# Kernel optimization log

Measured on AMD Instinct MI355X. Metric: run time of the kernel, lower is better.

## Reference

```python
import jax, jax.numpy as jnp
import numpy as np
from math import pi, log

B, H, W, C = 8, 128, 128, 3
N_LAT, D_LAT = 256, 512
DEPTH = 4
NUM_BANDS = 6
MAX_FREQ = 10.0
BASE = 2.0
CROSS_HEADS, CROSS_DH = 1, 64
LAT_HEADS, LAT_DH = 8, 64
FF_MULT = 4
INPUT_DIM = 2 * (2 * NUM_BANDS + 1) + C  # 29


def setup_inputs():
    ki = iter(jax.random.split(jax.random.key(0), 40))

    def nrm(shape, s=0.02):
        return jax.random.normal(next(ki), shape, jnp.float32) * s

    ic, il = CROSS_HEADS * CROSS_DH, LAT_HEADS * LAT_DH
    d, q = DEPTH, INPUT_DIM
    return {
        "x": jax.random.normal(next(ki), (B, D_LAT), jnp.float32),
        "latents": jax.random.normal(next(ki), (N_LAT, D_LAT), jnp.float32),
        "W_l2l": nrm((D_LAT, N_LAT * D_LAT)),
        "b_l2l": jnp.zeros((N_LAT * D_LAT,), jnp.float32),
        "ca_ln_q_g": jnp.ones((d, q)), "ca_ln_q_b": jnp.zeros((d, q)),
        "ca_ln_c_g": jnp.ones((d, D_LAT)), "ca_ln_c_b": jnp.zeros((d, D_LAT)),
        "ca_Wq": nrm((d, q, ic)), "ca_Wkv": nrm((d, D_LAT, 2 * ic)),
        "ca_Wo": nrm((d, ic, q)), "ca_bo": jnp.zeros((d, q)),
        "cf_ln_g": jnp.ones((d, q)), "cf_ln_b": jnp.zeros((d, q)),
        "cf_W1": nrm((d, q, q * FF_MULT * 2)), "cf_b1": jnp.zeros((d, q * FF_MULT * 2)),
        "cf_W2": nrm((d, q * FF_MULT, q)), "cf_b2": jnp.zeros((d, q)),
        "la_ln_g": jnp.ones((d, D_LAT)), "la_ln_b": jnp.zeros((d, D_LAT)),
        "la_Wq": nrm((d, D_LAT, il)), "la_Wkv": nrm((d, D_LAT, 2 * il)),
        "la_Wo": nrm((d, il, D_LAT)), "la_bo": jnp.zeros((d, D_LAT)),
        "lf_ln_g": jnp.ones((d, D_LAT)), "lf_ln_b": jnp.zeros((d, D_LAT)),
        "lf_W1": nrm((d, D_LAT, D_LAT * FF_MULT * 2)), "lf_b1": jnp.zeros((d, D_LAT * FF_MULT * 2)),
        "lf_W2": nrm((d, D_LAT * FF_MULT, D_LAT)), "lf_b2": jnp.zeros((d, D_LAT)),
    }


def _ln(t, g, b):
    m = jnp.mean(t, -1, keepdims=True)
    v = jnp.mean(jnp.square(t - m), -1, keepdims=True)
    return (t - m) * jax.lax.rsqrt(v + 1e-5) * g + b


def _attn(xq, ctx, Wq, Wkv, Wo, bo, heads):
    dh = Wq.shape[-1] // heads
    b, n, _ = xq.shape
    m = ctx.shape[1]
    qh = (xq @ Wq).reshape(b, n, heads, dh)
    k, v = jnp.split(ctx @ Wkv, 2, axis=-1)
    kh = k.reshape(b, m, heads, dh)
    vh = v.reshape(b, m, heads, dh)
    sim = jnp.einsum('bihd,bjhd->bhij', qh, kh) * (dh ** -0.5)
    attn = jax.nn.softmax(sim, axis=-1)
    out = jnp.einsum('bhij,bjhd->bihd', attn, vh).reshape(b, n, heads * dh)
    return out @ Wo + bo


def _geglu_ff(t, W1, b1, W2, b2):
    a, g = jnp.split(t @ W1 + b1, 2, axis=-1)
    return (a * jax.nn.gelu(g, approximate=False)) @ W2 + b2


def _forward(x, latents, W_l2l, b_l2l, ca_ln_q_g, ca_ln_q_b, ca_ln_c_g, ca_ln_c_b,
             ca_Wq, ca_Wkv, ca_Wo, ca_bo, cf_ln_g, cf_ln_b, cf_W1, cf_b1, cf_W2, cf_b2,
             la_ln_g, la_ln_b, la_Wq, la_Wkv, la_Wo, la_bo,
             lf_ln_g, lf_ln_b, lf_W1, lf_b1, lf_W2, lf_b2):
    # expand latent code to a set of latents and add learned latent array
    lat = (x @ W_l2l + b_l2l).reshape(B, N_LAT, D_LAT) + latents  # (B, N, D)

    # Fourier positional encoding of the output grid
    pos = jnp.stack(jnp.meshgrid(jnp.linspace(-1.0, 1.0, H), jnp.linspace(-1.0, 1.0, W), indexing='ij'), axis=-1)  # (H, W, 2)
    scales = BASE ** jnp.linspace(1.0, log(MAX_FREQ / 2) / log(BASE), NUM_BANDS)  # torch.logspace
    xp = pos[..., None] * scales * pi  # (H, W, 2, NUM_BANDS)
    enc = jnp.concatenate([jnp.sin(xp), jnp.cos(xp), pos[..., None]], axis=-1)  # (H, W, 2, 2B+1)
    enc = enc.reshape(H, W, 2 * (2 * NUM_BANDS + 1)).astype(jnp.float32)

    data = jnp.concatenate([jnp.zeros((B, H, W, C), jnp.float32),
                            jnp.broadcast_to(enc, (B, H, W, enc.shape[-1]))], axis=-1)
    data = data.reshape(B, H * W, INPUT_DIM)

    for i in range(DEPTH):
        ln_lat = _ln(lat, la_ln_g[i], la_ln_b[i])
        lat = lat + _attn(ln_lat, ln_lat, la_Wq[i], la_Wkv[i], la_Wo[i], la_bo[i], LAT_HEADS)
        lat = lat + _geglu_ff(_ln(lat, lf_ln_g[i], lf_ln_b[i]), lf_W1[i], lf_b1[i], lf_W2[i], lf_b2[i])
        qn = _ln(data, ca_ln_q_g[i], ca_ln_q_b[i])
        cn = _ln(lat, ca_ln_c_g[i], ca_ln_c_b[i])
        data = data + _attn(qn, cn, ca_Wq[i], ca_Wkv[i], ca_Wo[i], ca_bo[i], CROSS_HEADS)
        data = data + _geglu_ff(_ln(data, cf_ln_g[i], cf_ln_b[i]), cf_W1[i], cf_b1[i], cf_W2[i], cf_b2[i])

    return data[..., :C].reshape(B, H, W, C)


def reference(x, latents, W_l2l, b_l2l, ca_ln_q_g, ca_ln_q_b, ca_ln_c_g, ca_ln_c_b,
              ca_Wq, ca_Wkv, ca_Wo, ca_bo, cf_ln_g, cf_ln_b, cf_W1, cf_b1, cf_W2, cf_b2,
              la_ln_g, la_ln_b, la_Wq, la_Wkv, la_Wo, la_bo,
              lf_ln_g, lf_ln_b, lf_W1, lf_b1, lf_W2, lf_b2):
    return _forward(x, latents, W_l2l, b_l2l, ca_ln_q_g, ca_ln_q_b, ca_ln_c_g, ca_ln_c_b,
                    ca_Wq, ca_Wkv, ca_Wo, ca_bo, cf_ln_g, cf_ln_b, cf_W1, cf_b1, cf_W2, cf_b2,
                    la_ln_g, la_ln_b, la_Wq, la_Wkv, la_Wo, la_bo,
                    lf_ln_g, lf_ln_b, lf_W1, lf_b1, lf_W2, lf_b2)
```

## Files before the change

kernel.cpp:

```cpp
#include <hip/hip_runtime.h>
#include <math.h>

#define DEV __device__ __forceinline__
#define LSTRIDE 8537088

DEV float gelu_exact(float x){ return 0.5f*x*(1.0f+erff(x*0.70710678118654752440f)); }

DEV unsigned short f2bf(float x){
  union { float f; unsigned int u; } v; v.f = x;
  unsigned int r = v.u + 0x7FFFu + ((v.u >> 16) & 1u);
  return (unsigned short)(r >> 16);
}
DEV float bf2f(unsigned short b){ union { unsigned int u; float f; } v; v.u = ((unsigned int)b)<<16; return v.f; }
DEV void split2(float x, unsigned short& h, unsigned short& l){
  h = f2bf(x); l = f2bf(x - bf2f(h));
}

typedef __bf16 bf16x8 __attribute__((ext_vector_type(8)));
typedef float  f32x4  __attribute__((ext_vector_type(4)));

DEV void gload16(const void* g, void* lds){
  __builtin_amdgcn_global_load_lds((const __attribute__((address_space(1))) unsigned int*)g,
                                   (__attribute__((address_space(3))) unsigned int*)lds, 16, 0, 0);
}

__global__ __launch_bounds__(256) void k_encode(float* __restrict__ data)
{
  int p = blockIdx.x*256 + threadIdx.x;
  int hh = p >> 7, ww = p & 127;
  float y = -1.0f + hh*(2.0f/127.0f);
  float x = -1.0f + ww*(2.0f/127.0f);
  float e[26];
  #pragma unroll
  for (int i=0;i<6;i++){
    float sc = exp2f(1.0f + i*0.26438561897747245f) * 3.14159265358979323846f;
    e[i]     = sinf(y*sc);
    e[6+i]   = cosf(y*sc);
    e[13+i]  = sinf(x*sc);
    e[19+i]  = cosf(x*sc);
  }
  e[12]=y; e[25]=x;
  #pragma unroll
  for (int b=0;b<8;b++){
    float* dr = data + ((size_t)(b*16384 + p))*29;
    dr[0]=0.f; dr[1]=0.f; dr[2]=0.f;
    #pragma unroll
    for (int c=0;c<26;c++) dr[3+c]=e[c];
  }
}

__global__ __launch_bounds__(256) void k_l2l(const float* __restrict__ x,
    const float* __restrict__ Wl, const float* __restrict__ bl,
    const float* __restrict__ latents, float* __restrict__ lat)
{
  __shared__ float xs[8*512];
  int tid = threadIdx.x;
  for (int idx=tid; idx<4096; idx+=256) xs[idx]=x[idx];
  __syncthreads();
  int nIdx = blockIdx.x*256 + tid;
  float acc[8] = {0,0,0,0,0,0,0,0};
  for (int k=0;k<512;k++){
    float w = Wl[(size_t)k*131072 + nIdx];
    #pragma unroll
    for (int m=0;m<8;m++) acc[m] += xs[m*512+k]*w;
  }
  float add = bl[nIdx] + latents[nIdx];
  #pragma unroll
  for (int m=0;m<8;m++) lat[(size_t)m*131072 + nIdx] = acc[m] + add;
}

__global__ __launch_bounds__(256) void k_ln512s(const float* __restrict__ X,
    const float* __restrict__ g, const float* __restrict__ bv,
    unsigned short* __restrict__ hi, unsigned short* __restrict__ lo)
{
  __shared__ float red[8];
  int row = blockIdx.x, tid = threadIdx.x;
  const float* x = X + (size_t)row*512;
  float v0 = x[tid], v1 = x[tid+256];
  float s = v0+v1;
  #pragma unroll
  for (int off=32; off; off>>=1) s += __shfl_xor(s, off);
  if ((tid&63)==0) red[tid>>6] = s;
  __syncthreads();
  float mean = (red[0]+red[1]+red[2]+red[3]) * (1.0f/512.0f);
  float d0 = v0-mean, d1 = v1-mean;
  float q = d0*d0 + d1*d1;
  #pragma unroll
  for (int off=32; off; off>>=1) q += __shfl_xor(q, off);
  if ((tid&63)==0) red[4+(tid>>6)] = q;
  __syncthreads();
  float var = (red[4]+red[5]+red[6]+red[7]) * (1.0f/512.0f);
  float rstd = rsqrtf(var + 1e-5f);
  float y0 = d0*rstd*g[tid]     + bv[tid];
  float y1 = d1*rstd*g[tid+256] + bv[tid+256];
  unsigned short h,l;
  split2(y0,h,l); hi[(size_t)row*512+tid]=h;     lo[(size_t)row*512+tid]=l;
  split2(y1,h,l); hi[(size_t)row*512+tid+256]=h; lo[(size_t)row*512+tid+256]=l;
}

__global__ __launch_bounds__(256) void k_split_w(const float* __restrict__ W,
    unsigned short* __restrict__ hi, int K, int N)
{
  __shared__ float t[64][65];
  int z = blockIdx.z;
  W  += (size_t)z*K*N;
  hi += (size_t)z*LSTRIDE;
  unsigned short* lo = hi + (size_t)N*K;
  int k0 = blockIdx.x*64, n0 = blockIdx.y*64;
  int tid = threadIdx.x;
  #pragma unroll
  for (int i=0;i<4;i++){
    int s = tid + 256*i;
    int r = s >> 4, c4 = (s & 15)*4;
    float4 v = *(const float4*)&W[(size_t)(k0+r)*N + n0 + c4];
    t[r][c4+0]=v.x; t[r][c4+1]=v.y; t[r][c4+2]=v.z; t[r][c4+3]=v.w;
  }
  __syncthreads();
  #pragma unroll
  for (int i=0;i<4;i++){
    int s = tid + 256*i;
    int n = s >> 4, kc = (s & 15)*4;
    size_t o = (size_t)(n0+n)*K + k0 + kc;
    #pragma unroll
    for (int j=0;j<4;j++){
      unsigned short h,l; split2(t[kc+j][n], h, l);
      hi[o+j]=h; lo[o+j]=l;
    }
  }
}

__global__ __launch_bounds__(256) void k_prep_t(const float* __restrict__ src,
    unsigned short* __restrict__ dst, int K, int N, int Kd, int Nd)
{
  int z = blockIdx.z;
  src += (size_t)z*K*N;
  dst += (size_t)z*LSTRIDE;
  for (int idx = blockIdx.x*256 + threadIdx.x; idx < Nd*Kd; idx += gridDim.x*256){
    int n = idx / Kd, k = idx - n*Kd;
    float v = (k<K && n<N) ? src[(size_t)k*N + n] : 0.f;
    dst[idx] = f2bf(v);
  }
}

__global__ __launch_bounds__(256) void k_prep_w1(const float* __restrict__ W1,
    const float* __restrict__ b1, unsigned short* __restrict__ dst)
{
  int z = blockIdx.z;
  W1  += (size_t)z*6728;
  b1  += (size_t)z*232;
  dst += (size_t)z*LSTRIDE;
  float* b1r = (float*)(dst + 8192);
  for (int idx = blockIdx.x*256 + threadIdx.x; idx < 256*32; idx += gridDim.x*256){
    int n = idx >> 5, k = idx & 31;
    int f = n & 127, isg = n >> 7;
    float v = 0.f;
    if (f < 116 && k < 29) v = W1[(size_t)k*232 + isg*116 + f];
    dst[idx] = f2bf(v);
  }
  int n = blockIdx.x*256 + threadIdx.x;
  if (n < 256){
    int f = n & 127, isg = n >> 7;
    b1r[n] = (f < 116) ? b1[isg*116 + f] : 0.f;
  }
}

__global__ __launch_bounds__(256) void k_mfma(
    const unsigned short* __restrict__ Ahi, const unsigned short* __restrict__ Bhi,
    const float* __restrict__ bias, float* __restrict__ C,
    int M, int N, int K, int Ksplit, int accum)
{
  __shared__ unsigned short sm[4*128*32];
  int tid = threadIdx.x, lane = tid & 63, w = tid >> 6;
  int bm = blockIdx.x*128, bn = blockIdx.y*128;
  int Ks = K / Ksplit;
  int kbeg = blockIdx.z * Ks;
  const unsigned short* tsrc;
  if      (w==0) tsrc = Ahi + (size_t)bm*K;
  else if (w==1) tsrc = Ahi + (size_t)M*K + (size_t)bm*K;
  else if (w==2) tsrc = Bhi + (size_t)bn*K;
  else           tsrc = Bhi + (size_t)N*K + (size_t)bn*K;
  unsigned short* mylds = sm + w*4096;
  f32x4 acc[4][4];
  #pragma unroll
  for(int i=0;i<4;i++)
    #pragma unroll
    for(int j=0;j<4;j++) acc[i][j] = (f32x4){0.f,0.f,0.f,0.f};
  int wm = (w>>1)*64, wn = (w&1)*64;
  int frow = lane & 15, fq = lane >> 4;
  for (int k0 = kbeg; k0 < kbeg + Ks; k0 += 32){
    #pragma unroll
    for (int j=0;j<8;j++){
      int idx = j*64 + lane;
      int row = idx >> 2, qp = idx & 3;
      int q = (qp - row) & 3;
      gload16(tsrc + (size_t)row*K + k0 + q*8, mylds + j*512);
    }
    __syncthreads();
    bf16x8 ah[4], al[4];
    #pragma unroll
    for (int mt=0;mt<4;mt++){
      int row = wm + mt*16 + frow;
      int off = row*32 + ((fq + row)&3)*8;
      ah[mt] = *(const bf16x8*)(sm + off);
      al[mt] = *(const bf16x8*)(sm + 4096 + off);
    }
    #pragma unroll
    for (int nt=0;nt<4;nt++){
      int rowb = wn + nt*16 + frow;
      int offb = rowb*32 + ((fq + rowb)&3)*8;
      bf16x8 bh = *(const bf16x8*)(sm + 2*4096 + offb);
      bf16x8 bl = *(const bf16x8*)(sm + 3*4096 + offb);
      #pragma unroll
      for (int mt=0;mt<4;mt++){
        acc[mt][nt] = __builtin_amdgcn_mfma_f32_16x16x32_bf16(ah[mt], bh, acc[mt][nt], 0,0,0);
        acc[mt][nt] = __builtin_amdgcn_mfma_f32_16x16x32_bf16(ah[mt], bl, acc[mt][nt], 0,0,0);
        acc[mt][nt] = __builtin_amdgcn_mfma_f32_16x16x32_bf16(al[mt], bh, acc[mt][nt], 0,0,0);
      }
    }
    __syncthreads();
  }
  size_t zoff = (size_t)blockIdx.z * ((size_t)M*N);
  #pragma unroll
  for (int mt=0;mt<4;mt++){
    #pragma unroll
    for (int nt=0;nt<4;nt++){
      int col = bn + wn + nt*16 + frow;
      float bv = (bias && blockIdx.z==0) ? bias[col] : 0.f;
      #pragma unroll
      for (int r=0;r<4;r++){
        int row = bm + wm + mt*16 + fq*4 + r;
        float v = acc[mt][nt][r] + bv;
        if (accum) atomicAdd(&C[(size_t)row*N + col], v);
        else       C[zoff + (size_t)row*N + col] = v;
      }
    }
  }
}

__global__ __launch_bounds__(256) void k_mfma_glu(
    const unsigned short* __restrict__ Ahi, const unsigned short* __restrict__ Whi,
    const float* __restrict__ b1, unsigned short* __restrict__ Ghi,
    unsigned short* __restrict__ Glo)
{
  __shared__ unsigned short sm[16384];
  int tid = threadIdx.x, lane = tid & 63, w = tid >> 6;
  int bm = blockIdx.x*128, bnp = blockIdx.y*64;
  const unsigned short* Alo = Ahi + (size_t)2048*512;
  const unsigned short* Wlo = Whi + (size_t)4096*512;
  f32x4 aa[4][2], ag[4][2];
  #pragma unroll
  for (int i=0;i<4;i++)
    #pragma unroll
    for (int j=0;j<2;j++){ aa[i][j]=(f32x4){0.f,0.f,0.f,0.f}; ag[i][j]=(f32x4){0.f,0.f,0.f,0.f}; }
  int wm = (w>>1)*64, wnp = (w&1)*32;
  int frow = lane & 15, fq = lane >> 4;
  for (int k0=0;k0<512;k0+=32){
    #pragma unroll
    for (int j=0;j<8;j++){
      int c0 = w*512 + j*64;
      int c  = c0 + lane;
      int sel = c0 >> 8;
      const unsigned short* src; int wi;
      if (sel < 4){
        src = (sel < 2 ? Ahi : Alo) + (size_t)bm*512;
        wi = c & 511;
      } else {
        const unsigned short* wb = (sel < 6) ? Whi : Wlo;
        int cb = bnp + ((sel & 1) ? 2048 : 0);
        src = wb + (size_t)cb*512;
        wi = c & 255;
      }
      int row = wi >> 2, qp = wi & 3;
      int q = (qp - row) & 3;
      gload16(src + (size_t)row*512 + k0 + q*8, sm + c0*8);
    }
    __syncthreads();
    bf16x8 ah[4], al[4];
    #pragma unroll
    for (int mt=0;mt<4;mt++){
      int r = wm + mt*16 + frow;
      int off = r*32 + ((fq + r)&3)*8;
      ah[mt] = *(const bf16x8*)(sm + off);
      al[mt] = *(const bf16x8*)(sm + 4096 + off);
    }
    #pragma unroll
    for (int nt=0;nt<2;nt++){
      int rb = wnp + nt*16 + frow;
      int offb = rb*32 + ((fq + rb)&3)*8;
      bf16x8 bah = *(const bf16x8*)(sm +  8192 + offb);
      bf16x8 bgh = *(const bf16x8*)(sm + 10240 + offb);
      bf16x8 bal = *(const bf16x8*)(sm + 12288 + offb);
      bf16x8 bgl = *(const bf16x8*)(sm + 14336 + offb);
      #pragma unroll
      for (int mt=0;mt<4;mt++){
        aa[mt][nt] = __builtin_amdgcn_mfma_f32_16x16x32_bf16(ah[mt], bah, aa[mt][nt], 0,0,0);
        aa[mt][nt] = __builtin_amdgcn_mfma_f32_16x16x32_bf16(ah[mt], bal, aa[mt][nt], 0,0,0);
        aa[mt][nt] = __builtin_amdgcn_mfma_f32_16x16x32_bf16(al[mt], bah, aa[mt][nt], 0,0,0);
        ag[mt][nt] = __builtin_amdgcn_mfma_f32_16x16x32_bf16(ah[mt], bgh, ag[mt][nt], 0,0,0);
        ag[mt][nt] = __builtin_amdgcn_mfma_f32_16x16x32_bf16(ah[mt], bgl, ag[mt][nt], 0,0,0);
        ag[mt][nt] = __builtin_amdgcn_mfma_f32_16x16x32_bf16(al[mt], bgh, ag[mt][nt], 0,0,0);
      }
    }
    __syncthreads();
  }
  #pragma unroll
  for (int mt=0;mt<4;mt++){
    #pragma unroll
    for (int nt=0;nt<2;nt++){
      int col = bnp + wnp + nt*16 + frow;
      float ba = b1[col], bg = b1[2048+col];
      #pragma unroll
      for (int r=0;r<4;r++){
        int row = bm + wm + mt*16 + fq*4 + r;
        float av = aa[mt][nt][r] + ba;
        float gv = ag[mt][nt][r] + bg;
        unsigned short h,l; split2(av*gelu_exact(gv), h, l);
// ... 54 lines not shown
      for (int j=0;j<8;j++) v[j] = (__bf16)qp[kt*32 + j];
      aq[kt]=v;
    }
  } else {
    const unsigned short* qp = (const unsigned short*)Qv + (size_t)qrow*q_rs + h*64 + g*8;
    aq[0] = *(const bf16x8*)(qp);
    aq[1] = *(const bf16x8*)(qp + 32);
  }
  const unsigned short* kbb = Kb + ((size_t)bh*256 + l15)*64 + g*8;
  f32x4 sc[16];
  #pragma unroll
  for (int nt=0;nt<16;nt++) sc[nt] = (f32x4){0.f,0.f,0.f,0.f};
  #pragma unroll
  for (int nt=0;nt<16;nt++){
    bf16x8 b0 = *(const bf16x8*)(kbb + (size_t)nt*1024);
    bf16x8 b1 = *(const bf16x8*)(kbb + (size_t)nt*1024 + 32);
    sc[nt] = __builtin_amdgcn_mfma_f32_16x16x32_bf16(aq[0], b0, sc[nt], 0,0,0);
    sc[nt] = __builtin_amdgcn_mfma_f32_16x16x32_bf16(aq[1], b1, sc[nt], 0,0,0);
  }
  float mx[4] = {-1e30f,-1e30f,-1e30f,-1e30f};
  #pragma unroll
  for (int nt=0;nt<16;nt++)
    #pragma unroll
    for (int r=0;r<4;r++){ float v = sc[nt][r]*scale; sc[nt][r]=v; mx[r]=fmaxf(mx[r],v); }
  #pragma unroll
  for (int r=0;r<4;r++){
    #pragma unroll
    for (int m=1;m<16;m<<=1) mx[r] = fmaxf(mx[r], __shfl_xor(mx[r], m));
  }
  float sum[4] = {0.f,0.f,0.f,0.f};
  #pragma unroll
  for (int nt=0;nt<16;nt++)
    #pragma unroll
    for (int r=0;r<4;r++){ float e = __expf(sc[nt][r]-mx[r]); sc[nt][r]=e; sum[r]+=e; }
  #pragma unroll
  for (int r=0;r<4;r++){
    #pragma unroll
    for (int m=1;m<16;m<<=1) sum[r] += __shfl_xor(sum[r], m);
  }
  f32x4 o[4];
  #pragma unroll
  for (int nd=0;nd<4;nd++) o[nd] = (f32x4){0.f,0.f,0.f,0.f};
  unsigned short* pw = Pw + w*640;
  const unsigned short* vb  = Vthi + ((size_t)bh*64 + l15)*256 + g*8;
  const unsigned short* vbl = SPLITV ? (Vtlo + ((size_t)bh*64 + l15)*256 + g*8) : (const unsigned short*)0;
  #pragma unroll
  for (int kt=0;kt<8;kt++){
    __builtin_amdgcn_wave_barrier();
    #pragma unroll
    for (int t2=0;t2<2;t2++){
      int nt = kt*2 + t2;
      #pragma unroll
      for (int r=0;r<4;r++)
        pw[(g*4+r)*40 + t2*16 + l15] = f2bf(sc[nt][r]);
    }
    __builtin_amdgcn_wave_barrier();
    bf16x8 ap = *(const bf16x8*)(pw + l15*40 + g*8);
    #pragma unroll
    for (int nd=0;nd<4;nd++){
      bf16x8 bv = *(const bf16x8*)(vb + (size_t)nd*4096 + kt*32);
      o[nd] = __builtin_amdgcn_mfma_f32_16x16x32_bf16(ap, bv, o[nd], 0,0,0);
      if (SPLITV){
        bf16x8 bl = *(const bf16x8*)(vbl + (size_t)nd*4096 + kt*32);
        o[nd] = __builtin_amdgcn_mfma_f32_16x16x32_bf16(ap, bl, o[nd], 0,0,0);
      }
    }
  }
  float inv[4];
  #pragma unroll
  for (int r=0;r<4;r++) inv[r] = 1.0f/sum[r];
  int orow0 = b*nper + q0;
  #pragma unroll
  for (int nd=0;nd<4;nd++){
    #pragma unroll
    for (int r=0;r<4;r++){
      float v = o[nd][r]*inv[r];
      size_t off = (size_t)(orow0 + g*4 + r)*o_rs + h*64 + nd*16 + l15;
      if (OSPLIT){ unsigned short hh,ll; split2(v,hh,ll); O0[off]=hh; O1[off]=ll; }
      else O0[off] = f2bf(v);
    }
  }
}

__global__ __launch_bounds__(256) void k_qproj_f(const float* __restrict__ X,
    const float* __restrict__ lng, const float* __restrict__ lnb,
    const unsigned short* __restrict__ Wt, unsigned short* __restrict__ Out)
{
  __shared__ __align__(16) unsigned short sm[128*40];
  int tid = threadIdx.x;
  int row0b = blockIdx.x*128;
  if (tid < 128){
    const float* x = X + (size_t)(row0b + tid)*29;
    float a[29]; float s = 0.f;
    #pragma unroll
    for (int k=0;k<29;k++){ a[k]=x[k]; s+=a[k]; }
    float mean = s*(1.0f/29.0f);
    float qv = 0.f;
    #pragma unroll
    for (int k=0;k<29;k++){ float d=a[k]-mean; qv+=d*d; }
    float rstd = rsqrtf(qv*(1.0f/29.0f) + 1e-5f);
    unsigned short yb[32] __attribute__((aligned(16)));
    #pragma unroll
    for (int k=0;k<29;k++) yb[k] = f2bf((a[k]-mean)*rstd*lng[k] + lnb[k]);
    yb[29]=0; yb[30]=0; yb[31]=0;
    uint4* d4 = (uint4*)(sm + tid*40);
    const uint4* s4 = (const uint4*)yb;
    d4[0]=s4[0]; d4[1]=s4[1]; d4[2]=s4[2]; d4[3]=s4[3];
  }
  __syncthreads();
  int lane = tid & 63, w = tid >> 6;
  int l15 = lane & 15, gq = lane >> 4;
  int rw = w*32;
  bf16x8 a0 = *(const bf16x8*)(sm + (rw + l15)*40 + gq*8);
  bf16x8 a1 = *(const bf16x8*)(sm + (rw + 16 + l15)*40 + gq*8);
  f32x4 acc[2][4];
  #pragma unroll
  for (int mt=0;mt<2;mt++)
    #pragma unroll
    for (int nt=0;nt<4;nt++) acc[mt][nt] = (f32x4){0.f,0.f,0.f,0.f};
  #pragma unroll
  for (int nt=0;nt<4;nt++){
    bf16x8 bw = *(const bf16x8*)(Wt + (size_t)(nt*16 + l15)*32 + gq*8);
    acc[0][nt] = __builtin_amdgcn_mfma_f32_16x16x32_bf16(a0, bw, acc[0][nt], 0,0,0);
    acc[1][nt] = __builtin_amdgcn_mfma_f32_16x16x32_bf16(a1, bw, acc[1][nt], 0,0,0);
  }
  #pragma unroll
  for (int mt=0;mt<2;mt++)
    #pragma unroll
    for (int nt=0;nt<4;nt++)
      #pragma unroll
      for (int r=0;r<4;r++)
        Out[(size_t)(row0b + rw + mt*16 + gq*4 + r)*64 + nt*16 + l15] = f2bf(acc[mt][nt][r]);
}

__global__ __launch_bounds__(256) void k_nsmall(const unsigned short* __restrict__ A,
    const unsigned short* __restrict__ Wt, const float* __restrict__ bias,
    float* __restrict__ C, int K)
{
  int tid = threadIdx.x, lane = tid & 63, w = tid >> 6;
  int l15 = lane & 15, g = lane >> 4;
  int row0 = blockIdx.x*128 + w*32;
  f32x4 acc[2][2];
  #pragma unroll
  for (int mt=0;mt<2;mt++)
    #pragma unroll
    for (int nt=0;nt<2;nt++) acc[mt][nt] = (f32x4){0.f,0.f,0.f,0.f};
  for (int kt=0; kt<K; kt+=32){
    bf16x8 a0 = *(const bf16x8*)(A + (size_t)(row0 + l15)*K + kt + g*8);
    bf16x8 a1 = *(const bf16x8*)(A + (size_t)(row0 + 16 + l15)*K + kt + g*8);
    #pragma unroll
    for (int nt=0;nt<2;nt++){
      bf16x8 bw = *(const bf16x8*)(Wt + (size_t)(nt*16 + l15)*K + kt + g*8);
      acc[0][nt] = __builtin_amdgcn_mfma_f32_16x16x32_bf16(a0, bw, acc[0][nt], 0,0,0);
      acc[1][nt] = __builtin_amdgcn_mfma_f32_16x16x32_bf16(a1, bw, acc[1][nt], 0,0,0);
    }
  }
  #pragma unroll
  for (int mt=0;mt<2;mt++)
    #pragma unroll
    for (int nt=0;nt<2;nt++){
      int col = nt*16 + l15;
      if (col < 29){
        #pragma unroll
        for (int r=0;r<4;r++){
          size_t off = (size_t)(row0 + mt*16 + g*4 + r)*29 + col;
          C[off] += acc[mt][nt][r] + bias[col];
        }
      }
    }
}

__global__ __launch_bounds__(256) void k_ff1_f(const float* __restrict__ X,
    const float* __restrict__ lng, const float* __restrict__ lnb,
    const unsigned short* __restrict__ Wt, const float* __restrict__ b1r,
    unsigned short* __restrict__ G)
{
  __shared__ __align__(16) unsigned short sm[128*40];
  int tid = threadIdx.x;
  int row0b = blockIdx.x*128;
  if (tid < 128){
    const float* x = X + (size_t)(row0b + tid)*29;
    float a[29]; float s = 0.f;
    #pragma unroll
    for (int k=0;k<29;k++){ a[k]=x[k]; s+=a[k]; }
    float mean = s*(1.0f/29.0f);
    float qv = 0.f;
    #pragma unroll
    for (int k=0;k<29;k++){ float d=a[k]-mean; qv+=d*d; }
    float rstd = rsqrtf(qv*(1.0f/29.0f) + 1e-5f);
    unsigned short yb[32] __attribute__((aligned(16)));
    #pragma unroll
    for (int k=0;k<29;k++) yb[k] = f2bf((a[k]-mean)*rstd*lng[k] + lnb[k]);
    yb[29]=0; yb[30]=0; yb[31]=0;
    uint4* d4 = (uint4*)(sm + tid*40);
    const uint4* s4 = (const uint4*)yb;
    d4[0]=s4[0]; d4[1]=s4[1]; d4[2]=s4[2]; d4[3]=s4[3];
  }
  __syncthreads();
  int lane = tid & 63, w = tid >> 6;
  int l15 = lane & 15, gq = lane >> 4;
  int rw = w*32;
  bf16x8 a0 = *(const bf16x8*)(sm + (rw + l15)*40 + gq*8);
  bf16x8 a1 = *(const bf16x8*)(sm + (rw + 16 + l15)*40 + gq*8);
  f32x4 acc[2][16];
  #pragma unroll
  for (int mt=0;mt<2;mt++)
    #pragma unroll
    for (int nt=0;nt<16;nt++) acc[mt][nt] = (f32x4){0.f,0.f,0.f,0.f};
  #pragma unroll
  for (int nt=0;nt<16;nt++){
    bf16x8 bw = *(const bf16x8*)(Wt + (size_t)(nt*16 + l15)*32 + gq*8);
    acc[0][nt] = __builtin_amdgcn_mfma_f32_16x16x32_bf16(a0, bw, acc[0][nt], 0,0,0);
    acc[1][nt] = __builtin_amdgcn_mfma_f32_16x16x32_bf16(a1, bw, acc[1][nt], 0,0,0);
  }
  #pragma unroll
  for (int mt=0;mt<2;mt++){
    #pragma unroll
    for (int t=0;t<8;t++){
      float ba = b1r[t*16 + l15];
      float bg = b1r[128 + t*16 + l15];
      #pragma unroll
      for (int r=0;r<4;r++){
        float av = acc[mt][t][r]   + ba;
        float gv = acc[mt][t+8][r] + bg;
        G[(size_t)(row0b + rw + mt*16 + gq*4 + r)*128 + t*16 + l15] = f2bf(av * gelu_exact(gv));
      }
    }
  }
}

__global__ __launch_bounds__(256) void k_out(const float* __restrict__ data, float* __restrict__ out)
{
  int idx = blockIdx.x*256 + threadIdx.x;
  int p = idx/3, c = idx - p*3;
  out[idx] = data[(size_t)p*29 + c];
}

extern "C" void kernel_launch(void* const* d_in, const int* in_sizes, int n_in,
                              void* d_out, int out_size, void* d_ws, size_t ws_size,
                              hipStream_t stream) {
  const float* x        = (const float*)d_in[0];
  const float* latents  = (const float*)d_in[1];
  const float* W_l2l    = (const float*)d_in[2];
  const float* b_l2l    = (const float*)d_in[3];
  const float* ca_ln_q_g= (const float*)d_in[4];
  const float* ca_ln_q_b= (const float*)d_in[5];
  const float* ca_ln_c_g= (const float*)d_in[6];
  const float* ca_ln_c_b= (const float*)d_in[7];
  const float* ca_Wq    = (const float*)d_in[8];
  const float* ca_Wkv   = (const float*)d_in[9];
  const float* ca_Wo    = (const float*)d_in[10];
  const float* ca_bo    = (const float*)d_in[11];
  const float* cf_ln_g  = (const float*)d_in[12];
  const float* cf_ln_b  = (const float*)d_in[13];
  const float* cf_W1    = (const float*)d_in[14];
  const float* cf_b1    = (const float*)d_in[15];
  const float* cf_W2    = (const float*)d_in[16];
  const float* cf_b2    = (const float*)d_in[17];
  const float* la_ln_g  = (const float*)d_in[18];
  const float* la_ln_b  = (const float*)d_in[19];
  const float* la_Wq    = (const float*)d_in[20];
  const float* la_Wkv   = (const float*)d_in[21];
  const float* la_Wo    = (const float*)d_in[22];
  const float* la_bo    = (const float*)d_in[23];
  const float* lf_ln_g  = (const float*)d_in[24];
  const float* lf_ln_b  = (const float*)d_in[25];
  const float* lf_W1    = (const float*)d_in[26];
  const float* lf_b1    = (const float*)d_in[27];
  const float* lf_W2    = (const float*)d_in[28];
  const float* lf_b2    = (const float*)d_in[29];

  float* ws = (float*)d_ws;
  float* data = ws;
  float* lat  = ws + 3801088;
  unsigned short* latn_hi = (unsigned short*)(ws + 4849664);
  unsigned short* latn_lo = latn_hi + 1048576;
  float* I    = ws + 5898240;
  float* kv_c = ws + 20578304;
  unsigned short* Kb_c = (unsigned short*)(ws + 21626880);
  unsigned short* Vt_c = Kb_c + 131072;
  unsigned short* wsp  = (unsigned short*)(ws + 21757952);
  float* q_l  = I;
  float* kv_l = I + 1048576;
  unsigned short* Kb_l   = (unsigned short*)(I + 3145728);
  unsigned short* Vthi_l = Kb_l + 1048576;
  unsigned short* Vtlo_l = Vthi_l + 1048576;
  unsigned short* ao_hi  = (unsigned short*)(I + 4718592);
  unsigned short* ao_lo  = ao_hi + 1048576;
  unsigned short* gg_hi = (unsigned short*)(I + 8388608);
  unsigned short* gg_lo = gg_hi + 4194304;
  unsigned short* q_c  = (unsigned short*)(I + 2097152);
  unsigned short* gg_c = (unsigned short*)(I + 6291456);

  k_encode<<<64, 256, 0, stream>>>(data);
  k_l2l   <<<512, 256, 0, stream>>>(x, W_l2l, b_l2l, latents, lat);

  k_split_w<<<dim3(8,8,4),  256,0,stream>>>(la_Wq,  wsp,          512, 512);
  k_split_w<<<dim3(8,16,4), 256,0,stream>>>(la_Wkv, wsp+524288,   512, 1024);
  k_split_w<<<dim3(8,8,4),  256,0,stream>>>(la_Wo,  wsp+1572864,  512, 512);
  k_split_w<<<dim3(8,64,4), 256,0,stream>>>(lf_W1,  wsp+2097152,  512, 4096);
  k_split_w<<<dim3(32,8,4), 256,0,stream>>>(lf_W2,  wsp+6291456,  2048, 512);
  k_split_w<<<dim3(8,2,4),  256,0,stream>>>(ca_Wkv, wsp+8388608,  512, 128);
  k_prep_t <<<dim3(4,1,4),256,0,stream>>>(ca_Wq, wsp+8519680, 29, 64, 32, 64);
  k_prep_t <<<dim3(4,1,4),256,0,stream>>>(ca_Wo, wsp+8521728, 64, 29, 64, 32);
  k_prep_t <<<dim3(8,1,4),256,0,stream>>>(cf_W2, wsp+8523776, 116, 29, 128, 32);
  k_prep_w1<<<dim3(32,1,4),256,0,stream>>>(cf_W1, cf_b1, wsp+8527872);

  for (int i=0;i<4;i++){
    unsigned short* wl = wsp + (size_t)i*LSTRIDE;
    unsigned short* wqt  = wl;
    unsigned short* wkvt = wl + 524288;
    unsigned short* wot  = wl + 1572864;
    unsigned short* w1t  = wl + 2097152;
    unsigned short* w2t  = wl + 6291456;
    unsigned short* cakvt= wl + 8388608;
    unsigned short* WqT  = wl + 8519680;
    unsigned short* WoT  = wl + 8521728;
    unsigned short* W2T  = wl + 8523776;
    unsigned short* W1rT = wl + 8527872;
    float* b1r = (float*)(wl + 8536064);

    k_ln512s<<<2048,256,0,stream>>>(lat, la_ln_g+i*512, la_ln_b+i*512, latn_hi, latn_lo);
    k_mfma<<<dim3(16,4,1),256,0,stream>>>(latn_hi, wqt,  nullptr, q_l,  2048, 512, 512, 1, 0);
    k_mfma<<<dim3(16,8,1),256,0,stream>>>(latn_hi, wkvt, nullptr, kv_l, 2048,1024, 512, 1, 0);
    k_kvprep<<<1024,256,0,stream>>>(kv_l, 1024, 0, 512, 8, 64, Kb_l, Vthi_l, Vtlo_l, 1, 0);
    k_attn_mf<1,1,1><<<256,256,0,stream>>>(q_l, Kb_l, Vthi_l, Vtlo_l, ao_hi, ao_lo,
                                           512, 512, 8, 256, 0.125f);
    k_mfma<<<dim3(16,4,2),256,0,stream>>>(ao_hi, wot, la_bo+i*512, lat, 2048, 512, 512, 2, 1);
    k_ln512s<<<2048,256,0,stream>>>(lat, lf_ln_g+i*512, lf_ln_b+i*512, latn_hi, latn_lo);
    k_mfma_glu<<<dim3(16,32),256,0,stream>>>(latn_hi, w1t, lf_b1+i*4096, gg_hi, gg_lo);
    k_mfma<<<dim3(16,4,4),256,0,stream>>>(gg_hi, w2t, lf_b2+i*512, lat, 2048, 512, 2048, 4, 1);
    k_ln512s<<<2048,256,0,stream>>>(lat, ca_ln_c_g+i*512, ca_ln_c_b+i*512, latn_hi, latn_lo);
    k_mfma<<<dim3(16,1,4),256,0,stream>>>(latn_hi, cakvt, nullptr, kv_c, 2048, 128, 512, 4, 0);
    k_kvprep<<<512,256,0,stream>>>(kv_c, 128, 0, 64, 1, 8, Kb_c, Vt_c, nullptr, 4, 262144);
    k_qproj_f<<<1024,256,0,stream>>>(data, ca_ln_q_g+i*29, ca_ln_q_b+i*29, WqT, q_c);
    k_attn_mf<0,0,0><<<2048,256,0,stream>>>(q_c, Kb_c, Vt_c, nullptr, q_c, nullptr,
                                            64, 64, 1, 16384, 0.125f);
    k_nsmall<<<1024,256,0,stream>>>(q_c, WoT, ca_bo+i*29, data, 64);
    k_ff1_f<<<1024,256,0,stream>>>(data, cf_ln_g+i*29, cf_ln_b+i*29, W1rT, b1r, gg_c);
    k_nsmall<<<1024,256,0,stream>>>(gg_c, W2T, cf_b2+i*29, data, 128);
  }

  k_out<<<1536,256,0,stream>>>(data, (float*)d_out);
}
```

Before: 1.939 ms.

## Fuse latent QKV projection with KV prep and fuse cross-attention/FF chains

Merges the latent Q and KV weight splits into one contiguous QKV matrix and computes it in a single MFMA kernel whose epilogue writes Q in fp32, K in bf16 and V transposed in split bf16 directly, removing the separate kvprep pass and the fp32 KV intermediate. The cross-attention query LN+projection, attention and output projection are fused into one kernel that keeps intermediates in LDS. The cross feed-forward GEGLU and second projection are fused likewise. This cuts launches and global round trips of intermediates, at the cost of more LDS per block and higher register pressure.

```diff
diff --git a/kernel.cpp b/kernel.cpp
--- a/kernel.cpp
+++ b/kernel.cpp
@@ -99,13 +99,13 @@
 }
 
 __global__ __launch_bounds__(256) void k_split_w(const float* __restrict__ W,
-    unsigned short* __restrict__ hi, int K, int N)
+    unsigned short* __restrict__ hi, int K, int N, int Ntot, int n0off)
 {
   __shared__ float t[64][65];
   int z = blockIdx.z;
   W  += (size_t)z*K*N;
   hi += (size_t)z*LSTRIDE;
-  unsigned short* lo = hi + (size_t)N*K;
+  unsigned short* lo = hi + (size_t)Ntot*K;
   int k0 = blockIdx.x*64, n0 = blockIdx.y*64;
   int tid = threadIdx.x;
   #pragma unroll
@@ -120,7 +120,7 @@
   for (int i=0;i<4;i++){
     int s = tid + 256*i;
     int n = s >> 4, kc = (s & 15)*4;
-    size_t o = (size_t)(n0+n)*K + k0 + kc;
+    size_t o = (size_t)(n0off + n0 + n)*K + k0 + kc;
     #pragma unroll
     for (int j=0;j<4;j++){
       unsigned short h,l; split2(t[kc+j][n], h, l);
@@ -232,6 +232,86 @@
         float v = acc[mt][nt][r] + bv;
         if (accum) atomicAdd(&C[(size_t)row*N + col], v);
         else       C[zoff + (size_t)row*N + col] = v;
+      }
+    }
+  }
+}
+
+__global__ __launch_bounds__(256) void k_mfma_qkv(
+    const unsigned short* __restrict__ Ahi, const unsigned short* __restrict__ Bhi,
+    float* __restrict__ qout, unsigned short* __restrict__ Kb,
+    unsigned short* __restrict__ Vthi, unsigned short* __restrict__ Vtlo,
+    int M, int N, int K)
+{
+  __shared__ unsigned short sm[4*128*32];
+  int tid = threadIdx.x, lane = tid & 63, w = tid >> 6;
+  int bm = blockIdx.x*128, bn = blockIdx.y*128;
+  const unsigned short* tsrc;
+  if      (w==0) tsrc = Ahi + (size_t)bm*K;
+  else if (w==1) tsrc = Ahi + (size_t)M*K + (size_t)bm*K;
+  else if (w==2) tsrc = Bhi + (size_t)bn*K;
+  else           tsrc = Bhi + (size_t)N*K + (size_t)bn*K;
+  unsigned short* mylds = sm + w*4096;
+  f32x4 acc[4][4];
+  #pragma unroll
+  for(int i=0;i<4;i++)
+    #pragma unroll
+    for(int j=0;j<4;j++) acc[i][j] = (f32x4){0.f,0.f,0.f,0.f};
+  int wm = (w>>1)*64, wn = (w&1)*64;
+  int frow = lane & 15, fq = lane >> 4;
+  for (int k0 = 0; k0 < K; k0 += 32){
+    #pragma unroll
+    for (int j=0;j<8;j++){
+      int idx = j*64 + lane;
+      int row = idx >> 2, qp = idx & 3;
+      int q = (qp - row) & 3;
+      gload16(tsrc + (size_t)row*K + k0 + q*8, mylds + j*512);
+    }
+    __syncthreads();
+    bf16x8 ah[4], al[4];
+    #pragma unroll
+    for (int mt=0;mt<4;mt++){
+      int row = wm + mt*16 + frow;
+      int off = row*32 + ((fq + row)&3)*8;
+      ah[mt] = *(const bf16x8*)(sm + off);
+      al[mt] = *(const bf16x8*)(sm + 4096 + off);
+    }
+    #pragma unroll
+    for (int nt=0;nt<4;nt++){
+      int rowb = wn + nt*16 + frow;
+      int offb = rowb*32 + ((fq + rowb)&3)*8;
+      bf16x8 bh = *(const bf16x8*)(sm + 2*4096 + offb);
+      bf16x8 bl = *(const bf16x8*)(sm + 3*4096 + offb);
+      #pragma unroll
+      for (int mt=0;mt<4;mt++){
+        acc[mt][nt] = __builtin_amdgcn_mfma_f32_16x16x32_bf16(ah[mt], bh, acc[mt][nt], 0,0,0);
+        acc[mt][nt] = __builtin_amdgcn_mfma_f32_16x16x32_bf16(ah[mt], bl, acc[mt][nt], 0,0,0);
+        acc[mt][nt] = __builtin_amdgcn_mfma_f32_16x16x32_bf16(al[mt], bh, acc[mt][nt], 0,0,0);
+      }
+    }
+    __syncthreads();
+  }
+  #pragma unroll
+  for (int mt=0;mt<4;mt++){
+    #pragma unroll
+    for (int nt=0;nt<4;nt++){
+      int col = bn + wn + nt*16 + frow;
+      #pragma unroll
+      for (int r=0;r<4;r++){
+        int row = bm + wm + mt*16 + fq*4 + r;
+        float v = acc[mt][nt][r];
+        int b = row >> 8, j = row & 255;
+        if (col < 512){
+          qout[(size_t)row*512 + col] = v;
+        } else if (col < 1024){
+          int kc = col - 512, h = kc >> 6, d = kc & 63;
+          Kb[((size_t)((b*8+h)*256 + j))*64 + d] = f2bf(v);
+        } else {
+          int vc = col - 1024, h = vc >> 6, d = vc & 63;
+          size_t idx = ((size_t)((b*8+h)*64 + d))*256 + j;
+          unsigned short hh,ll; split2(v,hh,ll);
+          Vthi[idx]=hh; Vtlo[idx]=ll;
+        }
       }
     }
   }
@@ -452,12 +532,156 @@
   }
 }
 
-__global__ __launch_bounds__(256) void k_qproj_f(const float* __restrict__ X,
-    const float* __restrict__ lng, const float* __restrict__ lnb,
-    const unsigned short* __restrict__ Wt, unsigned short* __restrict__ Out)
-{
-  __shared__ __align__(16) unsigned short sm[128*40];
-  int tid = threadIdx.x;
+__global__ __launch_bounds__(256) void k_cattn(
+    const float* __restrict__ X, const float* __restrict__ lng, const float* __restrict__ lnb,
+    const unsigned short* __restrict__ WqT, const unsigned short* __restrict__ Kb,
+    const unsigned short* __restrict__ Vt, const unsigned short* __restrict__ WoT,
+    const float* __restrict__ bo, float* __restrict__ C, float scale)
+{
+  __shared__ __align__(16) unsigned short qn[64*40];
+  __shared__ __align__(16) unsigned short qa[4][16*72];
+  int tid = threadIdx.x, lane = tid & 63, w = tid >> 6;
+  int l15 = lane & 15, g = lane >> 4;
+  int r0 = blockIdx.x*64;
+  int bh = r0 >> 14;
+  if (tid < 64){
+    const float* x = X + (size_t)(r0 + tid)*29;
+    float a[29]; float s = 0.f;
+    #pragma unroll
+    for (int k=0;k<29;k++){ a[k]=x[k]; s+=a[k]; }
+    float mean = s*(1.0f/29.0f);
+    float qv = 0.f;
+    #pragma unroll
+    for (int k=0;k<29;k++){ float d=a[k]-mean; qv+=d*d; }
+    float rstd = rsqrtf(qv*(1.0f/29.0f) + 1e-5f);
+    unsigned short yb[32] __attribute__((aligned(16)));
+    #pragma unroll
+    for (int k=0;k<29;k++) yb[k] = f2bf((a[k]-mean)*rstd*lng[k] + lnb[k]);
+    yb[29]=0; yb[30]=0; yb[31]=0;
+    uint4* d4 = (uint4*)(qn + tid*40);
+    const uint4* s4 = (const uint4*)yb;
+    d4[0]=s4[0]; d4[1]=s4[1]; d4[2]=s4[2]; d4[3]=s4[3];
+  }
+  __syncthreads();
+  int rw = w*16;
+  bf16x8 a0 = *(const bf16x8*)(qn + (rw + l15)*40 + g*8);
+  f32x4 qv4[4];
+  #pragma unroll
+  for (int nt=0;nt<4;nt++) qv4[nt] = (f32x4){0.f,0.f,0.f,0.f};
+  #pragma unroll
+  for (int nt=0;nt<4;nt++){
+    bf16x8 bw = *(const bf16x8*)(WqT + (size_t)(nt*16 + l15)*32 + g*8);
+    qv4[nt] = __builtin_amdgcn_mfma_f32_16x16x32_bf16(a0, bw, qv4[nt], 0,0,0);
+  }
+  unsigned short* pa = qa[w];
+  #pragma unroll
+  for (int nt=0;nt<4;nt++)
+    #pragma unroll
+    for (int r=0;r<4;r++)
+      pa[(g*4+r)*72 + nt*16 + l15] = f2bf(qv4[nt][r]);
+  __builtin_amdgcn_wave_barrier();
+  bf16x8 aq[2];
+  aq[0] = *(const bf16x8*)(pa + l15*72 + g*8);
+  aq[1] = *(const bf16x8*)(pa + l15*72 + 32 + g*8);
+  __builtin_amdgcn_wave_barrier();
+  const unsigned short* kbb = Kb + ((size_t)bh*256 + l15)*64 + g*8;
+  f32x4 sc[16];
+  #pragma unroll
+  for (int nt=0;nt<16;nt++) sc[nt] = (f32x4){0.f,0.f,0.f,0.f};
+  #pragma unroll
+  for (int nt=0;nt<16;nt++){
+    bf16x8 b0 = *(const bf16x8*)(kbb + (size_t)nt*1024);
+    bf16x8 b1 = *(const bf16x8*)(kbb + (size_t)nt*1024 + 32);
+    sc[nt] = __builtin_amdgcn_mfma_f32_16x16x32_bf16(aq[0], b0, sc[nt], 0,0,0);
+    sc[nt] = __builtin_amdgcn_mfma_f32_16x16x32_bf16(aq[1], b1, sc[nt], 0,0,0);
+  }
+  float mx[4] = {-1e30f,-1e30f,-1e30f,-1e30f};
+  #pragma unroll
+  for (int nt=0;nt<16;nt++)
+    #pragma unroll
+    for (int r=0;r<4;r++){ float v = sc[nt][r]*scale; sc[nt][r]=v; mx[r]=fmaxf(mx[r],v); }
+  #pragma unroll
+  for (int r=0;r<4;r++){
+    #pragma unroll
+    for (int m=1;m<16;m<<=1) mx[r] = fmaxf(mx[r], __shfl_xor(mx[r], m));
+  }
+  float sum[4] = {0.f,0.f,0.f,0.f};
+  #pragma unroll
+  for (int nt=0;nt<16;nt++)
+    #pragma unroll
+    for (int r=0;r<4;r++){ float e = __expf(sc[nt][r]-mx[r]); sc[nt][r]=e; sum[r]+=e; }
+  #pragma unroll
+  for (int r=0;r<4;r++){
+    #pragma unroll
+    for (int m=1;m<16;m<<=1) sum[r] += __shfl_xor(sum[r], m);
+  }
+  f32x4 o[4];
+  #pragma unroll
+  for (int nd=0;nd<4;nd++) o[nd] = (f32x4){0.f,0.f,0.f,0.f};
+  const unsigned short* vb = Vt + ((size_t)bh*64 + l15)*256 + g*8;
+  #pragma unroll
+  for (int kt=0;kt<8;kt++){
+    __builtin_amdgcn_wave_barrier();
+    #pragma unroll
+    for (int t2=0;t2<2;t2++){
+      int nt = kt*2 + t2;
+      #pragma unroll
+      for (int r=0;r<4;r++)
+        pa[(g*4+r)*40 + t2*16 + l15] = f2bf(sc[nt][r]);
+    }
+    __builtin_amdgcn_wave_barrier();
+    bf16x8 ap = *(const bf16x8*)(pa + l15*40 + g*8);
+    #pragma unroll
+    for (int nd=0;nd<4;nd++){
+      bf16x8 bv = *(const bf16x8*)(vb + (size_t)nd*4096 + kt*32);
+      o[nd] = __builtin_amdgcn_mfma_f32_16x16x32_bf16(ap, bv, o[nd], 0,0,0);
+    }
+  }
+  float inv[4];
+  #pragma unroll
+  for (int r=0;r<4;r++) inv[r] = 1.0f/sum[r];
+  __builtin_amdgcn_wave_barrier();
+  #pragma unroll
+  for (int nd=0;nd<4;nd++)
+    #pragma unroll
+    for (int r=0;r<4;r++)
+      pa[(g*4+r)*72 + nd*16 + l15] = f2bf(o[nd][r]*inv[r]);
+  __builtin_amdgcn_wave_barrier();
+  bf16x8 ao0 = *(const bf16x8*)(pa + l15*72 + g*8);
+  bf16x8 ao1 = *(const bf16x8*)(pa + l15*72 + 32 + g*8);
+  f32x4 c2[2];
+  #pragma unroll
+  for (int nt=0;nt<2;nt++) c2[nt] = (f32x4){0.f,0.f,0.f,0.f};
+  #pragma unroll
+  for (int nt=0;nt<2;nt++){
+    bf16x8 bw0 = *(const bf16x8*)(WoT + (size_t)(nt*16 + l15)*64 + g*8);
+    bf16x8 bw1 = *(const bf16x8*)(WoT + (size_t)(nt*16 + l15)*64 + 32 + g*8);
+    c2[nt] = __builtin_amdgcn_mfma_f32_16x16x32_bf16(ao0, bw0, c2[nt], 0,0,0);
+    c2[nt] = __builtin_amdgcn_mfma_f32_16x16x32_bf16(ao1, bw1, c2[nt], 0,0,0);
+  }
+  #pragma unroll
+  for (int nt=0;nt<2;nt++){
+    int col = nt*16 + l15;
+    if (col < 29){
+      #pragma unroll
+      for (int r=0;r<4;r++){
+        size_t off = (size_t)(r0 + rw + g*4 + r)*29 + col;
+        C[off] += c2[nt][r] + bo[col];
+      }
+    }
+  }
+}
+
+__global__ __launch_bounds__(256) void k_cff(
+    const float* __restrict__ X, const float* __restrict__ lng, const float* __restrict__ lnb,
+    const unsigned short* __restrict__ W1rT, const float* __restrict__ b1r,
+    const unsigned short* __restrict__ W2T, const float* __restrict__ b2,
+    float* __restrict__ C)
+{
+  __shared__ __align__(16) unsigned short sm1[128*40];
+  __shared__ __align__(16) unsigned short gga[4][32*136];
+  int tid = threadIdx.x, lane = tid & 63, w = tid >> 6;
+  int l15 = lane & 15, g = lane >> 4;
   int row0b = blockIdx.x*128;
   if (tid < 128){
     const float* x = X + (size_t)(row0b + tid)*29;
@@ -473,56 +697,55 @@
     #pragma unroll
     for (int k=0;k<29;k++) yb[k] = f2bf((a[k]-mean)*rstd*lng[k] + lnb[k]);
     yb[29]=0; yb[30]=0; yb[31]=0;
-    uint4* d4 = (uint4*)(sm + tid*40);
+    uint4* d4 = (uint4*)(sm1 + tid*40);
     const uint4* s4 = (const uint4*)yb;
     d4[0]=s4[0]; d4[1]=s4[1]; d4[2]=s4[2]; d4[3]=s4[3];
   }
   __syncthreads();
-  int lane = tid & 63, w = tid >> 6;
-  int l15 = lane & 15, gq = lane >> 4;
   int rw = w*32;
-  bf16x8 a0 = *(const bf16x8*)(sm + (rw + l15)*40 + gq*8);
-  bf16x8 a1 = *(const bf16x8*)(sm + (rw + 16 + l15)*40 + gq*8);
-  f32x4 acc[2][4];
+  bf16x8 a0 = *(const bf16x8*)(sm1 + (rw + l15)*40 + g*8);
+  bf16x8 a1 = *(const bf16x8*)(sm1 + (rw + 16 + l15)*40 + g*8);
+  f32x4 acc[2][16];
   #pragma unroll
   for (int mt=0;mt<2;mt++)
     #pragma unroll
-    for (int nt=0;nt<4;nt++) acc[mt][nt] = (f32x4){0.f,0.f,0.f,0.f};
-  #pragma unroll
-  for (int nt=0;nt<4;nt++){
-    bf16x8 bw = *(const bf16x8*)(Wt + (size_t)(nt*16 + l15)*32 + gq*8);
+    for (int nt=0;nt<16;nt++) acc[mt][nt] = (f32x4){0.f,0.f,0.f,0.f};
+  #pragma unroll
+  for (int nt=0;nt<16;nt++){
+    bf16x8 bw = *(const bf16x8*)(W1rT + (size_t)(nt*16 + l15)*32 + g*8);
     acc[0][nt] = __builtin_amdgcn_mfma_f32_16x16x32_bf16(a0, bw, acc[0][nt], 0,0,0);
     acc[1][nt] = __builtin_amdgcn_mfma_f32_16x16x32_bf16(a1, bw, acc[1][nt], 0,0,0);
   }
+  unsigned short* gg = gga[w];
+  #pragma unroll
+  for (int mt=0;mt<2;mt++){
+    #pragma unroll
+    for (int t=0;t<8;t++){
+      float ba = b1r[t*16 + l15];
+      float bg = b1r[128 + t*16 + l15];
+      #pragma unroll
+      for (int r=0;r<4;r++){
+        float av = acc[mt][t][r]   + ba;
+        float gv = acc[mt][t+8][r] + bg;
+        gg[(mt*16 + g*4 + r)*136 + t*16 + l15] = f2bf(av * gelu_exact(gv));
+      }
+    }
+  }
+  __builtin_amdgcn_wave_barrier();
+  f32x4 c2[2][2];
   #pragma unroll
   for (int mt=0;mt<2;mt++)
     #pragma unroll
-    for (int nt=0;nt<4;nt++)
-      #pragma unroll
-      for (int r=0;r<4;r++)
-        Out[(size_t)(row0b + rw + mt*16 + gq*4 + r)*64 + nt*16 + l15] = f2bf(acc[mt][nt][r]);
-}
-
-__global__ __launch_bounds__(256) void k_nsmall(const unsigned short* __restrict__ A,
-    const unsigned short* __restrict__ Wt, const float* __restrict__ bias,
-    float* __restrict__ C, int K)
-{
-  int tid = threadIdx.x, lane = tid & 63, w = tid >> 6;
-  int l15 = lane & 15, g = lane >> 4;
-  int row0 = blockIdx.x*128 + w*32;
-  f32x4 acc[2][2];
-  #pragma unroll
-  for (int mt=0;mt<2;mt++)
-    #pragma unroll
-    for (int nt=0;nt<2;nt++) acc[mt][nt] = (f32x4){0.f,0.f,0.f,0.f};
-  for (int kt=0; kt<K; kt+=32){
-    bf16x8 a0 = *(const bf16x8*)(A + (size_t)(row0 + l15)*K + kt + g*8);
-    bf16x8 a1 = *(const bf16x8*)(A + (size_t)(row0 + 16 + l15)*K + kt + g*8);
+    for (int nt=0;nt<2;nt++) c2[mt][nt] = (f32x4){0.f,0.f,0.f,0.f};
+  #pragma unroll
+  for (int kt=0;kt<4;kt++){
+    bf16x8 af0 = *(const bf16x8*)(gg + (size_t)(l15)*136 + kt*32 + g*8);
+    bf16x8 af1 = *(const bf16x8*)(gg + (size_t)(16 + l15)*136 + kt*32 + g*8);
     #pragma unroll
     for (int nt=0;nt<2;nt++){
-      bf16x8 bw = *(const bf16x8*)(Wt + (size_t)(nt*16 + l15)*K + kt + g*8);
-      acc[0][nt] = __builtin_amdgcn_mfma_f32_16x16x32_bf16(a0, bw, acc[0][nt], 0,0,0);
-      acc[1][nt] = __builtin_amdgcn_mfma_f32_16x16x32_bf16(a1, bw, acc[1][nt], 0,0,0);
+      bf16x8 bw = *(const bf16x8*)(W2T + (size_t)(nt*16 + l15)*128 + kt*32 + g*8);
+      c2[0][nt] = __builtin_amdgcn_mfma_f32_16x16x32_bf16(af0, bw, c2[0][nt], 0,0,0);
+      c2[1][nt] = __builtin_amdgcn_mfma_f32_16x16x32_bf16(af1, bw, c2[1][nt], 0,0,0);
     }
   }
   #pragma unroll
@@ -533,70 +756,11 @@
       if (col < 29){
         #pragma unroll
         for (int r=0;r<4;r++){
-          size_t off = (size_t)(row0 + mt*16 + g*4 + r)*29 + col;
-          C[off] += acc[mt][nt][r] + bias[col];
+          size_t off = (size_t)(row0b + rw + mt*16 + g*4 + r)*29 + col;
+          C[off] += c2[mt][nt][r] + b2[col];
         }
       }
     }
-}
-
-__global__ __launch_bounds__(256) void k_ff1_f(const float* __restrict__ X,
-    const float* __restrict__ lng, const float* __restrict__ lnb,
-    const unsigned short* __restrict__ Wt, const float* __restrict__ b1r,
-    unsigned short* __restrict__ G)
-{
-  __shared__ __align__(16) unsigned short sm[128*40];
-  int tid = threadIdx.x;
-  int row0b = blockIdx.x*128;
-  if (tid < 128){
-    const float* x = X + (size_t)(row0b + tid)*29;
-    float a[29]; float s = 0.f;
-    #pragma unroll
-    for (int k=0;k<29;k++){ a[k]=x[k]; s+=a[k]; }
-    float mean = s*(1.0f/29.0f);
-    float qv = 0.f;
-    #pragma unroll
-    for (int k=0;k<29;k++){ float d=a[k]-mean; qv+=d*d; }
-    float rstd = rsqrtf(qv*(1.0f/29.0f) + 1e-5f);
-    unsigned short yb[32] __attribute__((aligned(16)));
-    #pragma unroll
-    for (int k=0;k<29;k++) yb[k] = f2bf((a[k]-mean)*rstd*lng[k] + lnb[k]);
-    yb[29]=0; yb[30]=0; yb[31]=0;
-    uint4* d4 = (uint4*)(sm + tid*40);
-    const uint4* s4 = (const uint4*)yb;
-    d4[0]=s4[0]; d4[1]=s4[1]; d4[2]=s4[2]; d4[3]=s4[3];
-  }
-  __syncthreads();
-  int lane = tid & 63, w = tid >> 6;
-  int l15 = lane & 15, gq = lane >> 4;
-  int rw = w*32;
-  bf16x8 a0 = *(const bf16x8*)(sm + (rw + l15)*40 + gq*8);
-  bf16x8 a1 = *(const bf16x8*)(sm + (rw + 16 + l15)*40 + gq*8);
-  f32x4 acc[2][16];
-  #pragma unroll
-  for (int mt=0;mt<2;mt++)
-    #pragma unroll
-    for (int nt=0;nt<16;nt++) acc[mt][nt] = (f32x4){0.f,0.f,0.f,0.f};
-  #pragma unroll
-  for (int nt=0;nt<16;nt++){
-    bf16x8 bw = *(const bf16x8*)(Wt + (size_t)(nt*16 + l15)*32 + gq*8);
-    acc[0][nt] = __builtin_amdgcn_mfma_f32_16x16x32_bf16(a0, bw, acc[0][nt], 0,0,0);
-    acc[1][nt] = __builtin_amdgcn_mfma_f32_16x16x32_bf16(a1, bw, acc[1][nt], 0,0,0);
-  }
-  #pragma unroll
-  for (int mt=0;mt<2;mt++){
-    #pragma unroll
-    for (int t=0;t<8;t++){
-      float ba = b1r[t*16 + l15];
-      float bg = b1r[128 + t*16 + l15];
-      #pragma unroll
-      for (int r=0;r<4;r++){
-        float av = acc[mt][t][r]   + ba;
-        float gv = acc[mt][t+8][r] + bg;
-        G[(size_t)(row0b + rw + mt*16 + gq*4 + r)*128 + t*16 + l15] = f2bf(av * gelu_exact(gv));
-      }
-    }
-  }
 }
 
 __global__ __launch_bounds__(256) void k_out(const float* __restrict__ data, float* __restrict__ out)
@@ -651,7 +815,6 @@
   unsigned short* Vt_c = Kb_c + 131072;
   unsigned short* wsp  = (unsigned short*)(ws + 21757952);
   float* q_l  = I;
-  float* kv_l = I + 1048576;
   unsigned short* Kb_l   = (unsigned short*)(I + 3145728);
   unsigned short* Vthi_l = Kb_l + 1048576;
   unsigned short* Vtlo_l = Vthi_l + 1048576;
@@ -659,18 +822,16 @@
   unsigned short* ao_lo  = ao_hi + 1048576;
   unsigned short* gg_hi = (unsigned short*)(I + 8388608);
   unsigned short* gg_lo = gg_hi + 4194304;
-  unsigned short* q_c  = (unsigned short*)(I + 2097152);
-  unsigned short* gg_c = (unsigned short*)(I + 6291456);
 
   k_encode<<<64, 256, 0, stream>>>(data);
   k_l2l   <<<512, 256, 0, stream>>>(x, W_l2l, b_l2l, latents, lat);
 
-  k_split_w<<<dim3(8,8,4),  256,0,stream>>>(la_Wq,  wsp,          512, 512);
-  k_split_w<<<dim3(8,16,4), 256,0,stream>>>(la_Wkv, wsp+524288,   512, 1024);
-  k_split_w<<<dim3(8,8,4),  256,0,stream>>>(la_Wo,  wsp+1572864,  512, 512);
-  k_split_w<<<dim3(8,64,4), 256,0,stream>>>(lf_W1,  wsp+2097152,  512, 4096);
-  k_split_w<<<dim3(32,8,4), 256,0,stream>>>(lf_W2,  wsp+6291456,  2048, 512);
-  k_split_w<<<dim3(8,2,4),  256,0,stream>>>(ca_Wkv, wsp+8388608,  512, 128);
+  k_split_w<<<dim3(8,8,4),  256,0,stream>>>(la_Wq,  wsp,          512, 512, 1536, 0);
+  k_split_w<<<dim3(8,16,4), 256,0,stream>>>(la_Wkv, wsp,          512,1024, 1536, 512);
+  k_split_w<<<dim3(8,8,4),  256,0,stream>>>(la_Wo,  wsp+1572864,  512, 512,  512, 0);
+  k_split_w<<<dim3(8,64,4), 256,0,stream>>>(lf_W1,  wsp+2097152,  512,4096, 4096, 0);
+  k_split_w<<<dim3(32,8,4), 256,0,stream>>>(lf_W2,  wsp+6291456, 2048, 512,  512, 0);
+  k_split_w<<<dim3(8,2,4),  256,0,stream>>>(ca_Wkv, wsp+8388608,  512, 128,  128, 0);
   k_prep_t <<<dim3(4,1,4),256,0,stream>>>(ca_Wq, wsp+8519680, 29, 64, 32, 64);
   k_prep_t <<<dim3(4,1,4),256,0,stream>>>(ca_Wo, wsp+8521728, 64, 29, 64, 32);
   k_prep_t <<<dim3(8,1,4),256,0,stream>>>(cf_W2, wsp+8523776, 116, 29, 128, 32);
@@ -678,8 +839,7 @@
 
   for (int i=0;i<4;i++){
     unsigned short* wl = wsp + (size_t)i*LSTRIDE;
-    unsigned short* wqt  = wl;
-    unsigned short* wkvt = wl + 524288;
+    unsigned short* wqkvt= wl;
     unsigned short* wot  = wl + 1572864;
     unsigned short* w1t  = wl + 2097152;
     unsigned short* w2t  = wl + 6291456;
@@ -691,9 +851,8 @@
     float* b1r = (float*)(wl + 8536064);
 
     k_ln512s<<<2048,256,0,stream>>>(lat, la_ln_g+i*512, la_ln_b+i*512, latn_hi, latn_lo);
-    k_mfma<<<dim3(16,4,1),256,0,stream>>>(latn_hi, wqt,  nullptr, q_l,  2048, 512, 512, 1, 0);
-    k_mfma<<<dim3(16,8,1),256,0,stream>>>(latn_hi, wkvt, nullptr, kv_l, 2048,1024, 512, 1, 0);
-    k_kvprep<<<1024,256,0,stream>>>(kv_l, 1024, 0, 512, 8, 64, Kb_l, Vthi_l, Vtlo_l, 1, 0);
+    k_mfma_qkv<<<dim3(16,12),256,0,stream>>>(latn_hi, wqkvt, q_l, Kb_l, Vthi_l, Vtlo_l,
+                                             2048, 1536, 512);
     k_attn_mf<1,1,1><<<256,256,0,stream>>>(q_l, Kb_l, Vthi_l, Vtlo_l, ao_hi, ao_lo,
                                            512, 512, 8, 256, 0.125f);
     k_mfma<<<dim3(16,4,2),256,0,stream>>>(ao_hi, wot, la_bo+i*512, lat, 2048, 512, 512, 2, 1);
@@ -703,12 +862,10 @@
     k_ln512s<<<2048,256,0,stream>>>(lat, ca_ln_c_g+i*512, ca_ln_c_b+i*512, latn_hi, latn_lo);
     k_mfma<<<dim3(16,1,4),256,0,stream>>>(latn_hi, cakvt, nullptr, kv_c, 2048, 128, 512, 4, 0);
     k_kvprep<<<512,256,0,stream>>>(kv_c, 128, 0, 64, 1, 8, Kb_c, Vt_c, nullptr, 4, 262144);
-    k_qproj_f<<<1024,256,0,stream>>>(data, ca_ln_q_g+i*29, ca_ln_q_b+i*29, WqT, q_c);
-    k_attn_mf<0,0,0><<<2048,256,0,stream>>>(q_c, Kb_c, Vt_c, nullptr, q_c, nullptr,
-                                            64, 64, 1, 16384, 0.125f);
-    k_nsmall<<<1024,256,0,stream>>>(q_c, WoT, ca_bo+i*29, data, 64);
-    k_ff1_f<<<1024,256,0,stream>>>(data, cf_ln_g+i*29, cf_ln_b+i*29, W1rT, b1r, gg_c);
-    k_nsmall<<<1024,256,0,stream>>>(gg_c, W2T, cf_b2+i*29, data, 128);
+    k_cattn<<<2048,256,0,stream>>>(data, ca_ln_q_g+i*29, ca_ln_q_b+i*29, WqT,
+                                   Kb_c, Vt_c, WoT, ca_bo+i*29, data, 0.125f);
+    k_cff<<<1024,256,0,stream>>>(data, cf_ln_g+i*29, cf_ln_b+i*29, W1rT, b1r,
+                                 W2T, cf_b2+i*29, data);
   }
 
   k_out<<<1536,256,0,stream>>>(data, (float*)d_out);
```

Measured after the change: 1.863 ms. 1.04x faster.
